# Performance work log

Hardware: AMD Instinct MI355X
Metric: run time of the kernel (lower is better)

Reference implementation:

```python
import jax, jax.numpy as jnp
import numpy as np

HIDDEN = 1024   # hidden_dimensions (dim_in)
NUM_HEADS = 16
HEAD_DIM = 64   # dim_q == dim_k == output_dimensions per head
BATCH = 4
SEQ = 2048


def setup_inputs() -> dict:
    key = jax.random.key(0)
    ks = jax.random.split(key, 11)
    s = 1.0 / np.sqrt(HIDDEN)
    so = 1.0 / np.sqrt(NUM_HEADS * HEAD_DIM)
    return {
        "Q": jax.random.normal(ks[0], (BATCH, SEQ, HIDDEN), jnp.float32),
        "K": jax.random.normal(ks[1], (BATCH, SEQ, HIDDEN), jnp.float32),
        "V": jax.random.normal(ks[2], (BATCH, SEQ, HIDDEN), jnp.float32),
        # per-head projection weights stacked over the head axis
        "Wq": jax.random.uniform(ks[3], (NUM_HEADS, HIDDEN, HEAD_DIM), jnp.float32, -s, s),
        "bq": jax.random.uniform(ks[4], (NUM_HEADS, HEAD_DIM), jnp.float32, -s, s),
        "Wk": jax.random.uniform(ks[5], (NUM_HEADS, HIDDEN, HEAD_DIM), jnp.float32, -s, s),
        "bk": jax.random.uniform(ks[6], (NUM_HEADS, HEAD_DIM), jnp.float32, -s, s),
        "Wv": jax.random.uniform(ks[7], (NUM_HEADS, HIDDEN, HEAD_DIM), jnp.float32, -s, s),
        "bv": jax.random.uniform(ks[8], (NUM_HEADS, HEAD_DIM), jnp.float32, -s, s),
        # output projection: concat(num_heads*head_dim) -> hidden
        "Wo": jax.random.uniform(ks[9], (NUM_HEADS * HEAD_DIM, HIDDEN), jnp.float32, -so, so),
        "bo": jax.random.uniform(ks[10], (HIDDEN,), jnp.float32, -so, so),
    }


def reference(Q, K, V, Wq, bq, Wk, bk, Wv, bv, Wo, bo):
    # Per-head linear projections (batched over heads instead of Python loop)
    q = jnp.einsum("bsd,hdk->bhsk", Q, Wq) + bq[None, :, None, :]  # [B,H,S,dk]
    k = jnp.einsum("bsd,hdk->bhsk", K, Wk) + bk[None, :, None, :]
    v = jnp.einsum("bsd,hdk->bhsk", V, Wv) + bv[None, :, None, :]
    # Scaled dot-product attention
    scale = 1.0 / jnp.sqrt(jnp.asarray(k.shape[-1], q.dtype))
    scores = jnp.einsum("bhqk,bhsk->bhqs", q, k) * scale          # [B,H,S,S]
    attn = jax.nn.softmax(scores, axis=-1)
    o = jnp.einsum("bhqs,bhsk->bhqk", attn, v)                     # [B,H,S,dk]
    # Concatenate heads along the feature dim, then output linear
    B, H, S, dk = o.shape
    concat = jnp.transpose(o, (0, 2, 1, 3)).reshape(B, S, H * dk)  # [B,S,H*dk]
    return concat @ Wo + bo                                        # [B,S,HIDDEN]
```

## Files before the change

### kernel.cpp

```cpp
#include <hip/hip_runtime.h>
#include <hip/hip_bf16.h>
#include <stdint.h>

typedef unsigned short u16;
typedef uint32_t u32;
typedef __attribute__((ext_vector_type(4))) float f32x4;
typedef __attribute__((ext_vector_type(16))) float f32x16;
typedef __attribute__((ext_vector_type(8))) short s8v;
typedef __attribute__((ext_vector_type(4))) unsigned short u16x4;
typedef __attribute__((ext_vector_type(2))) uint32_t u32x2;

#define SCALE_Q 0.18033688f

union PU { s8v v; u32 w[4]; };

__device__ __forceinline__ u16 f2bf(float f) {
  union { float f; uint32_t u; } v; v.f = f;
  uint32_t r = v.u + 0x7fffu + ((v.u >> 16) & 1u);
  return (u16)(r >> 16);
}

__device__ __forceinline__ u32 pk2(float lo, float hi) {
  __hip_bfloat162 h = __float22bfloat162_rn(float2{lo, hi});
  union { __hip_bfloat162 h; u32 u; } c; c.h = h; return c.u;
}

__device__ __forceinline__ void gl16(const void* g, void* l) {
  __builtin_amdgcn_global_load_lds((const __attribute__((address_space(1))) u32*)g,
                                   (__attribute__((address_space(3))) u32*)l, 16, 0, 0);
}

#define BARRIER()  __builtin_amdgcn_s_barrier()
#define SCHEDB()   __builtin_amdgcn_sched_barrier(0)
#define SGB(m, n)  __builtin_amdgcn_sched_group_barrier((m), (n), 0)

__global__ __launch_bounds__(256) void k_conv3(const float* __restrict__ a, const float* __restrict__ b,
                                               const float* __restrict__ c, u16* __restrict__ oa,
                                               u16* __restrict__ ob, u16* __restrict__ oc) {
  int which = blockIdx.y;
  const float* in = which == 0 ? a : (which == 1 ? b : c);
  u16* out = which == 0 ? oa : (which == 1 ? ob : oc);
  int i = (blockIdx.x * 256 + threadIdx.x) * 4;
  float4 v = *(const float4*)(in + i);
  u16x4 o; o[0] = f2bf(v.x); o[1] = f2bf(v.y); o[2] = f2bf(v.z); o[3] = f2bf(v.w);
  *(u16x4*)(out + i) = o;
}

__global__ __launch_bounds__(256) void k_convW_t(const float* __restrict__ wq, const float* __restrict__ wk,
                                                 const float* __restrict__ wv, u16* __restrict__ oq,
                                                 u16* __restrict__ ok, u16* __restrict__ ov) {
  __shared__ float T[64][65];
  const int z = blockIdx.z, h = blockIdx.y, d0 = blockIdx.x * 64;
  const float* w = z == 0 ? wq : (z == 1 ? wk : wv);
  u16* o = z == 0 ? oq : (z == 1 ? ok : ov);
  const float scale = z == 0 ? SCALE_Q : 1.0f;
  const int t = threadIdx.x;
#pragma unroll
  for (int i = 0; i < 16; ++i) {
    int f = t + i * 256;
    T[f >> 6][f & 63] = w[(h * 1024 + d0 + (f >> 6)) * 64 + (f & 63)];
  }
  __syncthreads();
#pragma unroll
  for (int i = 0; i < 16; ++i) {
    int g = t + i * 256;
    o[(h * 64 + (g >> 6)) * 1024 + d0 + (g & 63)] = f2bf(T[g & 63][g >> 6] * scale);
  }
}

__global__ __launch_bounds__(256) void k_convWo_t(const float* __restrict__ w, u16* __restrict__ o) {
  __shared__ float T[64][65];
  const int n0 = blockIdx.x * 64, c0 = blockIdx.y * 64;
  const int t = threadIdx.x;
#pragma unroll
  for (int i = 0; i < 16; ++i) {
    int f = t + i * 256;
    T[f >> 6][f & 63] = w[(c0 + (f >> 6)) * 1024 + n0 + (f & 63)];
  }
  __syncthreads();
#pragma unroll
  for (int i = 0; i < 16; ++i) {
    int g = t + i * 256;
    o[(n0 + (g >> 6)) * 1024 + c0 + (g & 63)] = f2bf(T[g & 63][g >> 6]);
  }
}

__global__ __launch_bounds__(256) void k_gemm3(
    const u16* __restrict__ Aq, const u16* __restrict__ Ak, const u16* __restrict__ Av,
    const u16* __restrict__ Bq, const u16* __restrict__ Bk, const u16* __restrict__ Bv,
    const float* __restrict__ bqp, const float* __restrict__ bkp, const float* __restrict__ bvp,
    u16* __restrict__ oq, u16* __restrict__ ok, u16* __restrict__ ov) {
  constexpr int Kd = 1024, Nd = 1024;
  __shared__ alignas(16) u16 As[2][128 * 64];
  __shared__ alignas(16) u16 Bs[2][128 * 64];
  const int z = blockIdx.z;
  const u16* A = z == 0 ? Aq : (z == 1 ? Ak : Av);
  const u16* Bt = z == 0 ? Bq : (z == 1 ? Bk : Bv);
  const float* bias = z == 0 ? bqp : (z == 1 ? bkp : bvp);

  const int t = threadIdx.x;
  const int lane = t & 63;
  const int w = t >> 6;
  const int wm = w >> 1, wn = w & 1;
  const int lr = lane & 15, lg = lane >> 4;
  const long bm = blockIdx.x * 128, bn = blockIdx.y * 128;
  const int r8 = lane >> 3, c8 = lane & 7;
  const int chunk = c8 ^ r8;

  f32x4 acc[4][4] = {};
  const u16* Ap = A + (bm + w * 8 + r8) * (long)Kd + chunk * 8;
  const u16* Bp = Bt + (bn + w * 8 + r8) * (long)Kd + chunk * 8;

  auto GSTAGE = [&](u16* Asb, u16* Bsb, int kt) {
#pragma unroll
    for (int p = 0; p < 4; ++p) {
      gl16(Ap + (long)p * 32 * Kd + kt, Asb + (p * 32 + w * 8) * 64);
      gl16(Bp + (long)p * 32 * Kd + kt, Bsb + (p * 32 + w * 8) * 64);
    }
  };
  auto GCOMP = [&](const u16* Asb, const u16* Bsb) {
#pragma unroll
    for (int ks = 0; ks < 2; ++ks) {
      s8v af[4], bf[4];
#pragma unroll
      for (int i = 0; i < 4; ++i) {
        int arow = wm * 64 + i * 16 + lr;
        af[i] = *(const s8v*)(Asb + arow * 64 + (((ks * 4 + lg) ^ (arow & 7)) * 8));
        int brow = wn * 64 + i * 16 + lr;
        bf[i] = *(const s8v*)(Bsb + brow * 64 + (((ks * 4 + lg) ^ (brow & 7)) * 8));
      }
#pragma unroll
      for (int i = 0; i < 4; ++i)
#pragma unroll
        for (int j = 0; j < 4; ++j)
          acc[i][j] = __builtin_amdgcn_mfma_f32_16x16x32_bf16(af[i], bf[j], acc[i][j], 0, 0, 0);
    }
  };

  GSTAGE(As[0], Bs[0], 0);
  for (int kt = 0; kt < 16; ++kt) {
    BARRIER();
    SCHEDB();
    if (kt < 15) {
      GSTAGE(As[(kt + 1) & 1], Bs[(kt + 1) & 1], (kt + 1) * 64);
      asm volatile("s_waitcnt vmcnt(8)" ::: "memory");
    } else {
      asm volatile("s_waitcnt vmcnt(0)" ::: "memory");
    }
    SCHEDB();
    BARRIER();
    SCHEDB();
    GCOMP(As[kt & 1], Bs[kt & 1]);
  }

  const float bscale = z == 0 ? SCALE_Q : 1.0f;
  float bcol[4];
#pragma unroll
  for (int j = 0; j < 4; ++j) bcol[j] = bias[bn + wn * 64 + j * 16 + lr] * bscale;

  if (z < 2) {
    u16* C = z == 0 ? oq : ok;
#pragma unroll
    for (int i = 0; i < 4; ++i) {
      long m0 = bm + wm * 64 + i * 16 + lg * 4;
#pragma unroll
      for (int j = 0; j < 4; ++j) {
        long n = bn + wn * 64 + j * 16 + lr;
#pragma unroll
        for (int r = 0; r < 4; ++r)
          C[(m0 + r) * Nd + n] = f2bf(acc[i][j][r] + bcol[j]);
      }
    }
  } else {
    u16* C = ov;
    int lgp = ((lg & 1) << 1) | (lg >> 1);
#pragma unroll
    for (int i = 0; i < 4; ++i) {
      long m0 = bm + wm * 64 + i * 16 + lgp * 4;
      int b = (int)(m0 >> 11), s0 = (int)(m0 & 2047);
#pragma unroll
      for (int j = 0; j < 4; ++j) {
        int n = (int)(bn + wn * 64 + j * 16 + lr);
        int h = n >> 6, dv = n & 63;
        u32x2 cc;
        cc[0] = pk2(acc[i][j][0] + bcol[j], acc[i][j][1] + bcol[j]);
        cc[1] = pk2(acc[i][j][2] + bcol[j], acc[i][j][3] + bcol[j]);
        *(u32x2*)(C + (long)((b * 16 + h) * 64 + dv) * 2048 + s0) = cc;
      }
    }
  }
}

__global__ __launch_bounds__(256) void k_gemmo(const u16* __restrict__ A, const u16* __restrict__ Bt,
                                               const float* __restrict__ bias, float* __restrict__ C) {
  constexpr int Kd = 1024, Nd = 1024;
  __shared__ alignas(16) u16 As[2][128 * 64];
  __shared__ alignas(16) u16 Bs[2][128 * 64];
  const int t = threadIdx.x;
  const int lane = t & 63;
  const int w = t >> 6;
  const int wm = w >> 1, wn = w & 1;
  const int lr = lane & 15, lg = lane >> 4;
  const long bm = blockIdx.x * 128, bn = blockIdx.y * 128;
  const int r8 = lane >> 3, c8 = lane & 7;
  const int chunk = c8 ^ r8;

  f32x4 acc[4][4] = {};
  const u16* Ap = A + (bm + w * 8 + r8) * (long)Kd + chunk * 8;
  const u16* Bp = Bt + (bn + w * 8 + r8) * (long)Kd + chunk * 8;

  auto GSTAGE = [&](u16* Asb, u16* Bsb, int kt) {
#pragma unroll
    for (int p = 0; p < 4; ++p) {
      gl16(Ap + (long)p * 32 * Kd + kt, Asb + (p * 32 + w * 8) * 64);
      gl16(Bp + (long)p * 32 * Kd + kt, Bsb + (p * 32 + w * 8) * 64);
    }
  };
  auto GCOMP = [&](const u16* Asb, const u16* Bsb) {
#pragma unroll
    for (int ks = 0; ks < 2; ++ks) {
      s8v af[4], bf[4];
#pragma unroll
      for (int i = 0; i < 4; ++i) {
        int arow = wm * 64 + i * 16 + lr;
        af[i] = *(const s8v*)(Asb + arow * 64 + (((ks * 4 + lg) ^ (arow & 7)) * 8));
        int brow = wn * 64 + i * 16 + lr;
        bf[i] = *(const s8v*)(Bsb + brow * 64 + (((ks * 4 + lg) ^ (brow & 7)) * 8));
      }
#pragma unroll
      for (int i = 0; i < 4; ++i)
#pragma unroll
        for (int j = 0; j < 4; ++j)
          acc[i][j] = __builtin_amdgcn_mfma_f32_16x16x32_bf16(af[i], bf[j], acc[i][j], 0, 0, 0);
    }
  };

  GSTAGE(As[0], Bs[0], 0);
  for (int kt = 0; kt < 16; ++kt) {
    BARRIER();
    SCHEDB();
    if (kt < 15) {
      GSTAGE(As[(kt + 1) & 1], Bs[(kt + 1) & 1], (kt + 1) * 64);
      asm volatile("s_waitcnt vmcnt(8)" ::: "memory");
    } else {
      asm volatile("s_waitcnt vmcnt(0)" ::: "memory");
    }
    SCHEDB();
    BARRIER();
    SCHEDB();
    GCOMP(As[kt & 1], Bs[kt & 1]);
  }

  float bcol[4];
#pragma unroll
  for (int j = 0; j < 4; ++j) bcol[j] = bias[bn + wn * 64 + j * 16 + lr];
#pragma unroll
  for (int i = 0; i < 4; ++i) {
    long m0 = bm + wm * 64 + i * 16 + lg * 4;
#pragma unroll
    for (int j = 0; j < 4; ++j) {
      long n = bn + wn * 64 + j * 16 + lr;
#pragma unroll
      for (int r = 0; r < 4; ++r)
        C[(m0 + r) * Nd + n] = acc[i][j][r] + bcol[j];
    }
  }
}

__global__ __launch_bounds__(256, 2) void k_attn(const u16* __restrict__ q, const u16* __restrict__ k,
                                                 const u16* __restrict__ vT, u16* __restrict__ o) {
  __shared__ alignas(16) u16 Ks[4][32 * 64];
  __shared__ alignas(16) u16 Vs[4][64 * 32];
  const int t = threadIdx.x;
  const int lane = t & 63;
  const int wv = t >> 6;
  const int l5 = lane & 31, hi = lane >> 5;
  const int r8 = lane >> 3, c8 = lane & 7;

  const int wg = blockIdx.x;
  const int ob = (wg & 7) * 64 + (wg >> 3);
  const int qt = ob & 7, h = (ob >> 3) & 15, b = ob >> 7;

  const int qrow0 = qt * 256 + wv * 64 + l5;
  const u16* qpA = q + ((long)(b * 2048 + qrow0) * 1024 + h * 64);
  const u16* qpB = qpA + 32 * 1024;
  s8v qfA[4], qfB[4];
#pragma unroll
  for (int s = 0; s < 4; ++s) {
    qfA[s] = *(const s8v*)(qpA + s * 16 + hi * 8);
    qfB[s] = *(const s8v*)(qpB + s * 16 + hi * 8);
  }

  const u16* Kst = k + (long)b * 2048 * 1024 + h * 64 + (long)(wv * 8 + r8) * 1024 + ((c8 ^ r8) * 8);
  const int dvS = wv * 16 + (lane >> 2);
  const int ccS = (lane & 3) ^ ((dvS >> 1) & 3);
  const u16* Vst = vT + (long)(b * 16 + h) * 131072 + (long)dvS * 2048 + ccS * 8;

  int koff[4];
#pragma unroll
  for (int s = 0; s < 4; ++s) koff[s] = l5 * 64 + (((2 * s + hi) ^ (l5 & 7)) * 8);
  int voff[2][2];
#pragma unroll
  for (int dh = 0; dh < 2; ++dh)
#pragma unroll
    for (int s2 = 0; s2 < 2; ++s2) {
      int dv = dh * 32 + l5;
      voff[dh][s2] = dv * 32 + (((2 * s2 + hi) ^ ((dv >> 1) & 3)) * 8);
    }

  f32x16 accA0 = {}, accA1 = {}, accB0 = {}, accB1 = {};
  float lA = 0.f, lB = 0.f;

  auto STAGE = [&](int buf, int kv0) {
    gl16(Kst + (long)kv0 * 1024, &Ks[buf][(wv * 8) * 64]);
    gl16(Vst + kv0,              &Vs[buf][(wv * 16) * 32]);
  };

  auto QKL = [&](const u16* Ksb, f32x16& sA, f32x16& sB) {
    s8v kf[4];
#pragma unroll
    for (int s = 0; s < 4; ++s) kf[s] = *(const s8v*)(Ksb + koff[s]);
#pragma unroll
    for (int s = 0; s < 4; ++s) {
      sA = __builtin_amdgcn_mfma_f32_32x32x16_bf16(kf[s], qfA[s], sA, 0, 0, 0);
      sB = __builtin_amdgcn_mfma_f32_32x32x16_bf16(kf[s], qfB[s], sB, 0, 0, 0);
    }
  };

  auto FIN = [&](const u16* Vsb, const f32x16& sA, const f32x16& sB) {
    PU pA[2], pB[2];
#pragma unroll
    for (int r1 = 0; r1 < 4; ++r1) {
      float a0 = __builtin_amdgcn_exp2f(sA[4 * r1 + 0]);
      float a1 = __builtin_amdgcn_exp2f(sA[4 * r1 + 1]);
      float a2 = __builtin_amdgcn_exp2f(sA[4 * r1 + 2]);
      float a3 = __builtin_amdgcn_exp2f(sA[4 * r1 + 3]);
      lA += (a0 + a1) + (a2 + a3);
      pA[r1 >> 1].w[(r1 & 1) * 2 + 0] = pk2(a0, a1);
      pA[r1 >> 1].w[(r1 & 1) * 2 + 1] = pk2(a2, a3);
      float c0 = __builtin_amdgcn_exp2f(sB[4 * r1 + 0]);
      float c1 = __builtin_amdgcn_exp2f(sB[4 * r1 + 1]);
      float c2 = __builtin_amdgcn_exp2f(sB[4 * r1 + 2]);
      float c3 = __builtin_amdgcn_exp2f(sB[4 * r1 + 3]);
      lB += (c0 + c1) + (c2 + c3);
      pB[r1 >> 1].w[(r1 & 1) * 2 + 0] = pk2(c0, c1);
      pB[r1 >> 1].w[(r1 & 1) * 2 + 1] = pk2(c2, c3);
    }
#pragma unroll
    for (int s2 = 0; s2 < 2; ++s2) {
      s8v vf0 = *(const s8v*)(Vsb + voff[0][s2]);
      s8v vf1 = *(const s8v*)(Vsb + voff[1][s2]);
      accA0 = __builtin_amdgcn_mfma_f32_32x32x16_bf16(vf0, pA[s2].v, accA0, 0, 0, 0);
      accA1 = __builtin_amdgcn_mfma_f32_32x32x16_bf16(vf1, pA[s2].v, accA1, 0, 0, 0);
      accB0 = __builtin_amdgcn_mfma_f32_32x32x16_bf16(vf0, pB[s2].v, accB0, 0, 0, 0);
      accB1 = __builtin_amdgcn_mfma_f32_32x32x16_bf16(vf1, pB[s2].v, accB1, 0, 0, 0);
    }
  };

#define SGBCHAIN() do { _Pragma("unroll") \
    for (int g_ = 0; g_ < 8; ++g_) { SGB(0x100, 1); SGB(0x8, 2); SGB(0x2, 18); } } while (0)

  f32x16 sAE, sBE, sAO, sBO;

  STAGE(0, 0);
  STAGE(1, 32);
  asm volatile("s_waitcnt vmcnt(2)" ::: "memory");
  BARRIER();
  STAGE(2, 64);
  sAE = {}; sBE = {};
  QKL(Ks[0], sAE, sBE);

  for (int tt = 0; tt < 62; tt += 2) {
    asm volatile("s_waitcnt vmcnt(2) lgkmcnt(0)" ::: "memory");
    BARRIER();
    STAGE((tt + 3) & 3, (tt + 3) * 32);
    sAO = {}; sBO = {};
    QKL(Ks[(tt + 1) & 3], sAO, sBO);
    FIN(Vs[tt & 3], sAE, sBE);
    SGBCHAIN();
    asm volatile("s_waitcnt vmcnt(2) lgkmcnt(0)" ::: "memory");
    BARRIER();
    if (tt + 4 < 64) STAGE((tt + 4) & 3, (tt + 4) * 32);
    sAE = {}; sBE = {};
    QKL(Ks[(tt + 2) & 3], sAE, sBE);
    FIN(Vs[(tt + 1) & 3], sAO, sBO);
    SGBCHAIN();
  }
  asm volatile("s_waitcnt vmcnt(0) lgkmcnt(0)" ::: "memory");
  BARRIER();
  sAO = {}; sBO = {};
  QKL(Ks[63 & 3], sAO, sBO);
  FIN(Vs[62 & 3], sAE, sBE);
  SGBCHAIN();
  FIN(Vs[63 & 3], sAO, sBO);

  lA += __shfl_xor(lA, 32);
  lB += __shfl_xor(lB, 32);
  float iA = 1.0f / lA, iB = 1.0f / lB;
  u16* opA = o + ((long)(b * 2048 + qrow0) * 1024 + h * 64);
  u16* opB = opA + 32 * 1024;
#pragma unroll
  for (int kb = 0; kb < 2; ++kb) {
#pragma unroll
    for (int r1 = 0; r1 < 4; ++r1) {
      u32x2 ca, cb;
      float a0 = kb ? accA1[4 * r1 + 0] : accA0[4 * r1 + 0];
      float a1 = kb ? accA1[4 * r1 + 1] : accA0[4 * r1 + 1];
      float a2 = kb ? accA1[4 * r1 + 2] : accA0[4 * r1 + 2];
      float a3 = kb ? accA1[4 * r1 + 3] : accA0[4 * r1 + 3];
      ca[0] = pk2(a0 * iA, a1 * iA);
      ca[1] = pk2(a2 * iA, a3 * iA);
      *(u32x2*)(opA + kb * 32 + r1 * 8 + hi * 4) = ca;
      float b0v = kb ? accB1[4 * r1 + 0] : accB0[4 * r1 + 0];
      float b1v = kb ? accB1[4 * r1 + 1] : accB0[4 * r1 + 1];
      float b2v = kb ? accB1[4 * r1 + 2] : accB0[4 * r1 + 2];
      float b3v = kb ? accB1[4 * r1 + 3] : accB0[4 * r1 + 3];
      cb[0] = pk2(b0v * iB, b1v * iB);
      cb[1] = pk2(b2v * iB, b3v * iB);
      *(u32x2*)(opB + kb * 32 + r1 * 8 + hi * 4) = cb;
    }
  }
#undef SGBCHAIN
}

extern "C" void kernel_launch(void* const* d_in, const int* in_sizes, int n_in,
                              void* d_out, int out_size, void* d_ws, size_t ws_size,
                              hipStream_t stream) {
  const float* Q  = (const float*)d_in[0];
  const float* K  = (const float*)d_in[1];
  const float* V  = (const float*)d_in[2];
  const float* Wq = (const float*)d_in[3];
  const float* bq = (const float*)d_in[4];
  const float* Wk = (const float*)d_in[5];
  const float* bk = (const float*)d_in[6];
  const float* Wv = (const float*)d_in[7];
  const float* bvp = (const float*)d_in[8];
  const float* Wo = (const float*)d_in[9];
  const float* bo = (const float*)d_in[10];
  float* out = (float*)d_out;

  char* ws = (char*)d_ws;
  const size_t MB16 = (size_t)8192 * 1024 * 2;
  u16* Qb  = (u16*)(ws);
  u16* Kb  = (u16*)(ws + MB16);
  u16* Vb  = (u16*)(ws + 2 * MB16);
  u16* WqT = (u16*)(ws + 3 * MB16);
  u16* WkT = (u16*)(ws + 3 * MB16 + ((size_t)2 << 20));
  u16* WvT = (u16*)(ws + 3 * MB16 + ((size_t)4 << 20));
  u16* WoT = (u16*)(ws + 3 * MB16 + ((size_t)6 << 20));
  u16* qws = (u16*)(ws + 3 * MB16 + ((size_t)8 << 20));
  u16* kws = (u16*)(ws + 4 * MB16 + ((size_t)8 << 20));
  u16* vTs = (u16*)(ws + 5 * MB16 + ((size_t)8 << 20));
  u16* ows = Qb;

  k_conv3<<<dim3(8192, 3), 256, 0, stream>>>(Q, K, V, Qb, Kb, Vb);
  k_convW_t<<<dim3(16, 16, 3), 256, 0, stream>>>(Wq, Wk, Wv, WqT, WkT, WvT);
  k_convWo_t<<<dim3(16, 16), 256, 0, stream>>>(Wo, WoT);

  k_gemm3<<<dim3(64, 8, 3), 256, 0, stream>>>(Qb, Kb, Vb, WqT, WkT, WvT,
                                              bq, bk, bvp, qws, kws, vTs);

  k_attn<<<dim3(512), 256, 0, stream>>>(qws, kws, vTs, ows);

  k_gemmo<<<dim3(64, 8), 256, 0, stream>>>(ows, WoT, bo, out);
}
```

Before: 203.7 us.

## Halve attention rows per wave, double grid, drop software-pipelined QK/PV interleave

The attention kernel now assigns 32 query rows per wave (128 per block) instead of 64, doubling the grid to 1024 blocks and raising launch bounds to allow 4 blocks per CU. The hand-pipelined odd/even QK-then-softmax-PV schedule with sched_group_barrier chains is replaced by a simple per-tile loop with s_setprio around MFMA groups, relying on more resident waves for latency hiding. This lowers register pressure and improves occupancy, but each K/V tile loaded into LDS is now reused by half as many query rows, which doubles K/V traffic, and intra-wave overlap of exp with MFMA is lost.

Measured after the change: 208.9 us. 1.03x slower.

```diff
diff --git a/kernel.cpp b/kernel.cpp
--- a/kernel.cpp
+++ b/kernel.cpp
@@ -32,7 +32,6 @@
 
 #define BARRIER()  __builtin_amdgcn_s_barrier()
 #define SCHEDB()   __builtin_amdgcn_sched_barrier(0)
-#define SGB(m, n)  __builtin_amdgcn_sched_group_barrier((m), (n), 0)
 
 __global__ __launch_bounds__(256) void k_conv3(const float* __restrict__ a, const float* __restrict__ b,
                                                const float* __restrict__ c, u16* __restrict__ oa,
@@ -267,7 +266,7 @@
   }
 }
 
-__global__ __launch_bounds__(256, 2) void k_attn(const u16* __restrict__ q, const u16* __restrict__ k,
+__global__ __launch_bounds__(256, 4) void k_attn(const u16* __restrict__ q, const u16* __restrict__ k,
                                                  const u16* __restrict__ vT, u16* __restrict__ o) {
   __shared__ alignas(16) u16 Ks[4][32 * 64];
   __shared__ alignas(16) u16 Vs[4][64 * 32];
@@ -278,18 +277,14 @@
   const int r8 = lane >> 3, c8 = lane & 7;
 
   const int wg = blockIdx.x;
-  const int ob = (wg & 7) * 64 + (wg >> 3);
-  const int qt = ob & 7, h = (ob >> 3) & 15, b = ob >> 7;
-
-  const int qrow0 = qt * 256 + wv * 64 + l5;
-  const u16* qpA = q + ((long)(b * 2048 + qrow0) * 1024 + h * 64);
-  const u16* qpB = qpA + 32 * 1024;
-  s8v qfA[4], qfB[4];
-#pragma unroll
-  for (int s = 0; s < 4; ++s) {
-    qfA[s] = *(const s8v*)(qpA + s * 16 + hi * 8);
-    qfB[s] = *(const s8v*)(qpB + s * 16 + hi * 8);
-  }
+  const int ob = (wg & 7) * 128 + (wg >> 3);
+  const int qt = ob & 15, h = (ob >> 4) & 15, b = ob >> 8;
+
+  const int qrow = qt * 128 + wv * 32 + l5;
+  const u16* qp = q + ((long)(b * 2048 + qrow) * 1024 + h * 64);
+  s8v qf[4];
+#pragma unroll
+  for (int s = 0; s < 4; ++s) qf[s] = *(const s8v*)(qp + s * 16 + hi * 8);
 
   const u16* Kst = k + (long)b * 2048 * 1024 + h * 64 + (long)(wv * 8 + r8) * 1024 + ((c8 ^ r8) * 8);
   const int dvS = wv * 16 + (lane >> 2);
@@ -308,119 +303,83 @@
       voff[dh][s2] = dv * 32 + (((2 * s2 + hi) ^ ((dv >> 1) & 3)) * 8);
     }
 
-  f32x16 accA0 = {}, accA1 = {}, accB0 = {}, accB1 = {};
-  float lA = 0.f, lB = 0.f;
+  f32x16 acc0 = {}, acc1 = {};
+  float lsum = 0.f;
 
   auto STAGE = [&](int buf, int kv0) {
     gl16(Kst + (long)kv0 * 1024, &Ks[buf][(wv * 8) * 64]);
     gl16(Vst + kv0,              &Vs[buf][(wv * 16) * 32]);
   };
 
-  auto QKL = [&](const u16* Ksb, f32x16& sA, f32x16& sB) {
+  auto TILE = [&](int buf) {
+    const u16* Ksb = Ks[buf];
+    const u16* Vsb = Vs[buf];
     s8v kf[4];
 #pragma unroll
     for (int s = 0; s < 4; ++s) kf[s] = *(const s8v*)(Ksb + koff[s]);
-#pragma unroll
-    for (int s = 0; s < 4; ++s) {
-      sA = __builtin_amdgcn_mfma_f32_32x32x16_bf16(kf[s], qfA[s], sA, 0, 0, 0);
-      sB = __builtin_amdgcn_mfma_f32_32x32x16_bf16(kf[s], qfB[s], sB, 0, 0, 0);
-    }
-  };
-
-  auto FIN = [&](const u16* Vsb, const f32x16& sA, const f32x16& sB) {
-    PU pA[2], pB[2];
+    f32x16 sa = {};
+    __builtin_amdgcn_s_setprio(1);
+#pragma unroll
+    for (int s = 0; s < 4; ++s)
+      sa = __builtin_amdgcn_mfma_f32_32x32x16_bf16(kf[s], qf[s], sa, 0, 0, 0);
+    __builtin_amdgcn_s_setprio(0);
+    PU p[2];
 #pragma unroll
     for (int r1 = 0; r1 < 4; ++r1) {
-      float a0 = __builtin_amdgcn_exp2f(sA[4 * r1 + 0]);
-      float a1 = __builtin_amdgcn_exp2f(sA[4 * r1 + 1]);
-      float a2 = __builtin_amdgcn_exp2f(sA[4 * r1 + 2]);
-      float a3 = __builtin_amdgcn_exp2f(sA[4 * r1 + 3]);
-      lA += (a0 + a1) + (a2 + a3);
-      pA[r1 >> 1].w[(r1 & 1) * 2 + 0] = pk2(a0, a1);
-      pA[r1 >> 1].w[(r1 & 1) * 2 + 1] = pk2(a2, a3);
-      float c0 = __builtin_amdgcn_exp2f(sB[4 * r1 + 0]);
-      float c1 = __builtin_amdgcn_exp2f(sB[4 * r1 + 1]);
-      float c2 = __builtin_amdgcn_exp2f(sB[4 * r1 + 2]);
-      float c3 = __builtin_amdgcn_exp2f(sB[4 * r1 + 3]);
-      lB += (c0 + c1) + (c2 + c3);
-      pB[r1 >> 1].w[(r1 & 1) * 2 + 0] = pk2(c0, c1);
-      pB[r1 >> 1].w[(r1 & 1) * 2 + 1] = pk2(c2, c3);
-    }
+      float a0 = __builtin_amdgcn_exp2f(sa[4 * r1 + 0]);
+      float a1 = __builtin_amdgcn_exp2f(sa[4 * r1 + 1]);
+      float a2 = __builtin_amdgcn_exp2f(sa[4 * r1 + 2]);
+      float a3 = __builtin_amdgcn_exp2f(sa[4 * r1 + 3]);
+      lsum += (a0 + a1) + (a2 + a3);
+      p[r1 >> 1].w[(r1 & 1) * 2 + 0] = pk2(a0, a1);
+      p[r1 >> 1].w[(r1 & 1) * 2 + 1] = pk2(a2, a3);
+    }
+    s8v vf0[2], vf1[2];
 #pragma unroll
     for (int s2 = 0; s2 < 2; ++s2) {
-      s8v vf0 = *(const s8v*)(Vsb + voff[0][s2]);
-      s8v vf1 = *(const s8v*)(Vsb + voff[1][s2]);
-      accA0 = __builtin_amdgcn_mfma_f32_32x32x16_bf16(vf0, pA[s2].v, accA0, 0, 0, 0);
-      accA1 = __builtin_amdgcn_mfma_f32_32x32x16_bf16(vf1, pA[s2].v, accA1, 0, 0, 0);
-      accB0 = __builtin_amdgcn_mfma_f32_32x32x16_bf16(vf0, pB[s2].v, accB0, 0, 0, 0);
-      accB1 = __builtin_amdgcn_mfma_f32_32x32x16_bf16(vf1, pB[s2].v, accB1, 0, 0, 0);
-    }
-  };
-
-#define SGBCHAIN() do { _Pragma("unroll") \
-    for (int g_ = 0; g_ < 8; ++g_) { SGB(0x100, 1); SGB(0x8, 2); SGB(0x2, 18); } } while (0)
-
-  f32x16 sAE, sBE, sAO, sBO;
+      vf0[s2] = *(const s8v*)(Vsb + voff[0][s2]);
+      vf1[s2] = *(const s8v*)(Vsb + voff[1][s2]);
+    }
+    __builtin_amdgcn_s_setprio(1);
+#pragma unroll
+    for (int s2 = 0; s2 < 2; ++s2) {
+      acc0 = __builtin_amdgcn_mfma_f32_32x32x16_bf16(vf0[s2], p[s2].v, acc0, 0, 0, 0);
+      acc1 = __builtin_amdgcn_mfma_f32_32x32x16_bf16(vf1[s2], p[s2].v, acc1, 0, 0, 0);
+    }
+    __builtin_amdgcn_s_setprio(0);
+  };
 
   STAGE(0, 0);
   STAGE(1, 32);
-  asm volatile("s_waitcnt vmcnt(2)" ::: "memory");
-  BARRIER();
   STAGE(2, 64);
-  sAE = {}; sBE = {};
-  QKL(Ks[0], sAE, sBE);
-
-  for (int tt = 0; tt < 62; tt += 2) {
-    asm volatile("s_waitcnt vmcnt(2) lgkmcnt(0)" ::: "memory");
+  for (int tt = 0; tt < 64; ++tt) {
+    if (tt <= 61) asm volatile("s_waitcnt vmcnt(4) lgkmcnt(0)" ::: "memory");
+    else if (tt == 62) asm volatile("s_waitcnt vmcnt(2) lgkmcnt(0)" ::: "memory");
+    else asm volatile("s_waitcnt vmcnt(0) lgkmcnt(0)" ::: "memory");
+    SCHEDB();
     BARRIER();
-    STAGE((tt + 3) & 3, (tt + 3) * 32);
-    sAO = {}; sBO = {};
-    QKL(Ks[(tt + 1) & 3], sAO, sBO);
-    FIN(Vs[tt & 3], sAE, sBE);
-    SGBCHAIN();
-    asm volatile("s_waitcnt vmcnt(2) lgkmcnt(0)" ::: "memory");
-    BARRIER();
-    if (tt + 4 < 64) STAGE((tt + 4) & 3, (tt + 4) * 32);
-    sAE = {}; sBE = {};
-    QKL(Ks[(tt + 2) & 3], sAE, sBE);
-    FIN(Vs[(tt + 1) & 3], sAO, sBO);
-    SGBCHAIN();
-  }
-  asm volatile("s_waitcnt vmcnt(0) lgkmcnt(0)" ::: "memory");
-  BARRIER();
-  sAO = {}; sBO = {};
-  QKL(Ks[63 & 3], sAO, sBO);
-  FIN(Vs[62 & 3], sAE, sBE);
-  SGBCHAIN();
-  FIN(Vs[63 & 3], sAO, sBO);
-
-  lA += __shfl_xor(lA, 32);
-  lB += __shfl_xor(lB, 32);
-  float iA = 1.0f / lA, iB = 1.0f / lB;
-  u16* opA = o + ((long)(b * 2048 + qrow0) * 1024 + h * 64);
-  u16* opB = opA + 32 * 1024;
+    SCHEDB();
+    if (tt + 3 < 64) STAGE((tt + 3) & 3, (tt + 3) * 32);
+    TILE(tt & 3);
+  }
+
+  lsum += __shfl_xor(lsum, 32);
+  float inv = 1.0f / lsum;
+  u16* op = o + ((long)(b * 2048 + qrow) * 1024 + h * 64);
 #pragma unroll
   for (int kb = 0; kb < 2; ++kb) {
 #pragma unroll
     for (int r1 = 0; r1 < 4; ++r1) {
-      u32x2 ca, cb;
-      float a0 = kb ? accA1[4 * r1 + 0] : accA0[4 * r1 + 0];
-      float a1 = kb ? accA1[4 * r1 + 1] : accA0[4 * r1 + 1];
-      float a2 = kb ? accA1[4 * r1 + 2] : accA0[4 * r1 + 2];
-      float a3 = kb ? accA1[4 * r1 + 3] : accA0[4 * r1 + 3];
-      ca[0] = pk2(a0 * iA, a1 * iA);
-      ca[1] = pk2(a2 * iA, a3 * iA);
-      *(u32x2*)(opA + kb * 32 + r1 * 8 + hi * 4) = ca;
-      float b0v = kb ? accB1[4 * r1 + 0] : accB0[4 * r1 + 0];
-      float b1v = kb ? accB1[4 * r1 + 1] : accB0[4 * r1 + 1];
-      float b2v = kb ? accB1[4 * r1 + 2] : accB0[4 * r1 + 2];
-      float b3v = kb ? accB1[4 * r1 + 3] : accB0[4 * r1 + 3];
-      cb[0] = pk2(b0v * iB, b1v * iB);
-      cb[1] = pk2(b2v * iB, b3v * iB);
-      *(u32x2*)(opB + kb * 32 + r1 * 8 + hi * 4) = cb;
-    }
-  }
-#undef SGBCHAIN
+      u32x2 cc;
+      float a0 = kb ? acc1[4 * r1 + 0] : acc0[4 * r1 + 0];
+      float a1 = kb ? acc1[4 * r1 + 1] : acc0[4 * r1 + 1];
+      float a2 = kb ? acc1[4 * r1 + 2] : acc0[4 * r1 + 2];
+      float a3 = kb ? acc1[4 * r1 + 3] : acc0[4 * r1 + 3];
+      cc[0] = pk2(a0 * inv, a1 * inv);
+      cc[1] = pk2(a2 * inv, a3 * inv);
+      *(u32x2*)(op + kb * 32 + r1 * 8 + hi * 4) = cc;
+    }
+  }
 }
 
 extern "C" void kernel_launch(void* const* d_in, const int* in_sizes, int n_in,
@@ -460,7 +419,7 @@
   k_gemm3<<<dim3(64, 8, 3), 256, 0, stream>>>(Qb, Kb, Vb, WqT, WkT, WvT,
                                               bq, bk, bvp, qws, kws, vTs);
 
-  k_attn<<<dim3(512), 256, 0, stream>>>(qws, kws, vTs, ows);
+  k_attn<<<dim3(1024), 256, 0, stream>>>(qws, kws, vTs, ows);
 
   k_gemmo<<<dim3(64, 8), 256, 0, stream>>>(ows, WoT, bo, out);
 }
```
